# Performance work log

Measured on AMD Instinct MI355X. Metric: run time of the kernel, lower is better.

Reference implementation:

```python
import jax, jax.numpy as jnp
import numpy as np
from jax import lax

DIM = 96
HEADS = 6
H = W = D = 64
EPS = 1e-12  # torch F.normalize default


def setup_inputs() -> dict:
    key = jax.random.key(0)
    k1, k2, k3, k4 = jax.random.split(key, 4)
    x = jax.random.normal(k1, (1, DIM, H, W, D), dtype=jnp.float32)
    # qkv 1x1 conv weight, stored as (3*dim, dim) matrix
    w_qkv = jax.random.normal(k2, (3 * DIM, DIM), dtype=jnp.float32) * (1.0 / np.sqrt(DIM))
    # depthwise 3x3x3 conv weight (OIDHW with I=1, groups=3*dim)
    w_dw = jax.random.normal(k3, (3 * DIM, 1, 3, 3, 3), dtype=jnp.float32) * (1.0 / np.sqrt(27))
    # output 1x1 conv weight as (dim, dim)
    w_proj = jax.random.normal(k4, (DIM, DIM), dtype=jnp.float32) * (1.0 / np.sqrt(DIM))
    temperature = jnp.ones((HEADS, 1, 1), dtype=jnp.float32)
    return {"x": x, "w_qkv": w_qkv, "w_dw": w_dw, "w_proj": w_proj, "temperature": temperature}


def _l2norm(t):
    # torch F.normalize(dim=-1): t / max(||t||, eps)
    n = jnp.sqrt(jnp.sum(t * t, axis=-1, keepdims=True))
    return t / jnp.maximum(n, EPS)


def reference(x, w_qkv, w_dw, w_proj, temperature):
    b, c, h, w, d = x.shape
    ch = c // HEADS  # per-head channels
    # 1x1 conv -> pointwise GEMM over channels
    qkv = jnp.einsum('bchwd,oc->bohwd', x, w_qkv)  # (b, 3c, h, w, d)
    # depthwise 3x3x3 conv, padding 1
    qkv = lax.conv_general_dilated(
        qkv, w_dw, window_strides=(1, 1, 1), padding=[(1, 1)] * 3,
        feature_group_count=3 * c,
        dimension_numbers=('NCDHW', 'OIDHW', 'NCDHW'))
    q, k, v = jnp.split(qkv, 3, axis=1)
    n = h * w * d
    q = q.reshape(b, HEADS, ch, n)
    k = k.reshape(b, HEADS, ch, n)
    v = v.reshape(b, HEADS, ch, n)
    q = _l2norm(q)
    k = _l2norm(k)
    # channel-wise attention: (b, heads, ch, ch)
    attn = jnp.einsum('bhcn,bhdn->bhcd', q, k) * temperature[None]
    attn = jax.nn.softmax(attn, axis=-1)
    out = jnp.einsum('bhcd,bhdn->bhcn', attn, v)  # (b, heads, ch, n)
    out = out.reshape(b, c, h, w, d)
    out = jnp.einsum('bchwd,oc->bohwd', out, w_proj)
    return out
```

## Files before the change

### kernel.cpp

```cpp
#include <hip/hip_runtime.h>
#include <hip/hip_bf16.h>

#define NTOT 262144
typedef __hip_bfloat16 bf16;
typedef __attribute__((ext_vector_type(8))) short short8;
typedef __attribute__((ext_vector_type(4))) float f32x4;

__device__ inline ushort f2bf(float f){ bf16 b = __float2bfloat16(f); return *(ushort*)&b; }
__device__ inline float bf2f(ushort u){ union{unsigned i;float f;}v; v.i = (unsigned)u<<16; return v.f; }

__global__ void detect_dtype(const ushort* __restrict__ w, int* __restrict__ flag) {
  int tid = threadIdx.x;
  int sane = 0;
  for (int i = tid; i < 512; i += 64) {
    ushort u = w[2 * i];
    int e = (u >> 7) & 0xff;
    sane += (e == 0 || (e >= 100 && e <= 140)) ? 1 : 0;
  }
#pragma unroll
  for (int off = 32; off > 0; off >>= 1) sane += __shfl_down(sane, off, 64);
  if (tid == 0) *flag = (sane >= 256) ? 1 : 0;
}

__global__ void cvt_bf16(const void* __restrict__ in, ushort* __restrict__ outw,
                         int n, const int* __restrict__ flag) {
  int f = *flag;
  for (int i = blockIdx.x * 256 + threadIdx.x; i < n; i += gridDim.x * 256)
    outw[i] = f ? ((const ushort*)in)[i] : f2bf(((const float*)in)[i]);
}

template<int OF, bool DYNIN, bool DYNOUT>
__global__ __launch_bounds__(384)
void gemm96(const ushort* __restrict__ W, const void* __restrict__ X,
            void* __restrict__ C, const int* __restrict__ flag) {
  __shared__ __align__(16) ushort xs[64][104];
  const int tid = threadIdx.x;
  const long n0 = (long)blockIdx.x * 64;
  const int f = *flag;
  {
    int c = tid % 96, nq = tid / 96;
    ushort tmp[16];
    if (!DYNIN || f) {
      const ushort* xp = (const ushort*)X + (size_t)c * NTOT + n0 + nq * 16;
      uint4 a0 = *(const uint4*)xp;
      uint4 a1 = *(const uint4*)(xp + 8);
      const unsigned* aw = (const unsigned*)&a0;
#pragma unroll
      for (int i = 0; i < 4; i++) { tmp[2*i] = (ushort)(aw[i] & 0xffffu); tmp[2*i+1] = (ushort)(aw[i] >> 16); }
      const unsigned* aw1 = (const unsigned*)&a1;
#pragma unroll
      for (int i = 0; i < 4; i++) { tmp[8+2*i] = (ushort)(aw1[i] & 0xffffu); tmp[8+2*i+1] = (ushort)(aw1[i] >> 16); }
    } else {
      const float* xp = (const float*)X + (size_t)c * NTOT + n0 + nq * 16;
#pragma unroll
      for (int k = 0; k < 4; k++) {
        float4 v = *(const float4*)(xp + 4 * k);
        tmp[4*k+0] = f2bf(v.x); tmp[4*k+1] = f2bf(v.y);
        tmp[4*k+2] = f2bf(v.z); tmp[4*k+3] = f2bf(v.w);
      }
    }
    ushort* dst = &xs[nq * 16][c];
#pragma unroll
    for (int i = 0; i < 16; i++) dst[i * 104] = tmp[i];
  }
  __syncthreads();
  const int wave = tid >> 6, lane = tid & 63;
  const int col = lane & 15, quad = lane >> 4;
  f32x4 acc[OF][4];
#pragma unroll
  for (int a = 0; a < OF; a++)
#pragma unroll
    for (int b = 0; b < 4; b++) acc[a][b] = (f32x4)0.f;
  const int obase = wave * (16 * OF);
#pragma unroll
  for (int ks = 0; ks < 3; ks++) {
    short8 bfrag[4];
#pragma unroll
    for (int nf = 0; nf < 4; nf++)
      bfrag[nf] = *(const short8*)&xs[nf*16 + col][ks*32 + quad*8];
#pragma unroll
    for (int of = 0; of < OF; of++) {
      const int o = obase + of*16 + col;
      short8 afrag = *(const short8*)(W + (size_t)o * 96 + ks*32 + quad*8);
#pragma unroll
      for (int nf = 0; nf < 4; nf++)
        acc[of][nf] = __builtin_amdgcn_mfma_f32_16x16x32_bf16(afrag, bfrag[nf], acc[of][nf], 0, 0, 0);
    }
  }
#pragma unroll
  for (int of = 0; of < OF; of++)
#pragma unroll
    for (int nf = 0; nf < 4; nf++)
#pragma unroll
      for (int r = 0; r < 4; r++) {
        int o = obase + of*16 + quad*4 + r;
        long n = n0 + nf*16 + col;
        float v = acc[of][nf][r];
        if (!DYNOUT || f) ((ushort*)C)[(size_t)o * NTOT + n] = f2bf(v);
        else              ((float*) C)[(size_t)o * NTOT + n] = v;
      }
}

__global__ __launch_bounds__(256)
void dwconv3(const ushort* __restrict__ in, const void* __restrict__ wt,
             ushort* __restrict__ out, const int* __restrict__ flag) {
  const int c = blockIdx.z;
  const int tid = threadIdx.x;
  const int dq = tid & 7;
  const int w = blockIdx.y * 8 + ((tid >> 3) & 7);
  const int h = blockIdx.x * 4 + (tid >> 6);
  const int d0 = dq * 8;
  __shared__ float wsm[27];
  if (tid < 27) {
    int f = *flag;
    wsm[tid] = f ? bf2f(((const ushort*)wt)[c * 27 + tid])
                 : ((const float*)wt)[c * 27 + tid];
  }
  __syncthreads();
  float acc[8];
#pragma unroll
  for (int i = 0; i < 8; i++) acc[i] = 0.f;
  const size_t cbase = (size_t)c * NTOT;
#pragma unroll
  for (int dh = -1; dh <= 1; dh++) {
    int hh = h + dh;
    if (hh < 0 || hh > 63) continue;
#pragma unroll
    for (int dw = -1; dw <= 1; dw++) {
      int ww = w + dw;
      bool wok = (ww >= 0 && ww <= 63);
      uint4 va = make_uint4(0u, 0u, 0u, 0u);
      if (wok)
        va = *(const uint4*)(in + cbase + ((size_t)hh * 64 + ww) * 64 + d0);
      const unsigned* u = (const unsigned*)&va;
      float x0 = bf2f((ushort)(u[0] & 0xffffu)), x1 = bf2f((ushort)(u[0] >> 16));
      float x2 = bf2f((ushort)(u[1] & 0xffffu)), x3 = bf2f((ushort)(u[1] >> 16));
      float x4 = bf2f((ushort)(u[2] & 0xffffu)), x5 = bf2f((ushort)(u[2] >> 16));
      float x6 = bf2f((ushort)(u[3] & 0xffffu)), x7 = bf2f((ushort)(u[3] >> 16));
      float xlm = __shfl_up(x7, 1, 8);
      float xrm = __shfl_down(x0, 1, 8);
      float xl = (dq > 0) ? xlm : 0.f;
      float xr = (dq < 7) ? xrm : 0.f;
      const int wb = (dh + 1) * 9 + (dw + 1) * 3;
      float wL = wsm[wb], wC = wsm[wb + 1], wR = wsm[wb + 2];
      acc[0] += wL*xl + wC*x0 + wR*x1;
      acc[1] += wL*x0 + wC*x1 + wR*x2;
      acc[2] += wL*x1 + wC*x2 + wR*x3;
      acc[3] += wL*x2 + wC*x3 + wR*x4;
      acc[4] += wL*x3 + wC*x4 + wR*x5;
      acc[5] += wL*x4 + wC*x5 + wR*x6;
      acc[6] += wL*x5 + wC*x6 + wR*x7;
      acc[7] += wL*x6 + wC*x7 + wR*xr;
    }
  }
  ushort o8[8];
#pragma unroll
  for (int i = 0; i < 8; i++) o8[i] = f2bf(acc[i]);
  *(uint4*)(out + cbase + ((size_t)h * 64 + w) * 64 + d0) = *(uint4*)o8;
}

__global__ __launch_bounds__(256)
void gram16(const ushort* __restrict__ qk, float* __restrict__ G) {
  const int hd = blockIdx.y;
  const int tid = threadIdx.x, wave = tid >> 6, lane = tid & 63;
  const int col = lane & 15, quad = lane >> 4;
  const ushort* qp = qk + (size_t)(hd * 16 + col) * NTOT;
  const ushort* kp = qp + (size_t)96 * NTOT;
  f32x4 aqk = (f32x4)0.f, aqq = (f32x4)0.f, akk = (f32x4)0.f;
  const int nbase = blockIdx.x * 4096 + wave * 32 + quad * 8;
#pragma unroll 4
  for (int it = 0; it < 32; it++) {
    short8 qf = *(const short8*)(qp + nbase + it * 128);
    short8 kf = *(const short8*)(kp + nbase + it * 128);
    aqk = __builtin_amdgcn_mfma_f32_16x16x32_bf16(qf, kf, aqk, 0, 0, 0);
    aqq = __builtin_amdgcn_mfma_f32_16x16x32_bf16(qf, qf, aqq, 0, 0, 0);
    akk = __builtin_amdgcn_mfma_f32_16x16x32_bf16(kf, kf, akk, 0, 0, 0);
  }
  __shared__ float red[4][64][12];
#pragma unroll
  for (int r = 0; r < 4; r++) {
    red[wave][lane][r]     = aqk[r];
    red[wave][lane][4 + r] = aqq[r];
    red[wave][lane][8 + r] = akk[r];
  }
  __syncthreads();
  if (wave == 0) {
#pragma unroll
    for (int j = 0; j < 12; j++) {
      float v = red[0][lane][j] + red[1][lane][j] + red[2][lane][j] + red[3][lane][j];
      int sub = j >> 2, r = j & 3;
      atomicAdd(&G[hd * 768 + sub * 256 + (quad * 4 + r) * 16 + col], v);
    }
  }
}

__global__ __launch_bounds__(256)
void attn_mix(const float* __restrict__ G, const void* __restrict__ wp,
              const void* __restrict__ temp, ushort* __restrict__ M,
              const int* __restrict__ flag) {
  __shared__ float As[6][16][16];
  const int tid = threadIdx.x;
  const int f = *flag;
  if (tid < 96) {
    int hd = tid >> 4, c = tid & 15;
    const float* Gh = G + hd * 768;
    float qn = fmaxf(sqrtf(fmaxf(Gh[256 + c * 17], 0.f)), 1e-12f);
    float t = f ? bf2f(((const ushort*)temp)[hd]) : ((const float*)temp)[hd];
    float lg[16];
    float mx = -1e30f;
#pragma unroll
    for (int d = 0; d < 16; d++) {
      float kn = fmaxf(sqrtf(fmaxf(Gh[512 + d * 17], 0.f)), 1e-12f);
      lg[d] = Gh[c * 16 + d] / (qn * kn) * t;
      mx = fmaxf(mx, lg[d]);
    }
    float s = 0.f;
#pragma unroll
    for (int d = 0; d < 16; d++) { lg[d] = __expf(lg[d] - mx); s += lg[d]; }
    float inv = 1.f / s;
#pragma unroll
    for (int d = 0; d < 16; d++) As[hd][c][d] = lg[d] * inv;
  }
  __syncthreads();
  for (int i = 0; i < 36; i++) {
    int idx = tid + 256 * i;
    int o = idx / 96, p = idx - o * 96;
    int hd = p >> 4, d = p & 15;
    float s = 0.f;
#pragma unroll
    for (int cc = 0; cc < 16; cc++) {
      float wv = f ? bf2f(((const ushort*)wp)[o * 96 + hd * 16 + cc])
                   : ((const float*)wp)[o * 96 + hd * 16 + cc];
      s += wv * As[hd][cc][d];
    }
    M[idx] = f2bf(s);
  }
}

extern "C" void kernel_launch(void* const* d_in, const int* in_sizes, int n_in,
                              void* d_out, int out_size, void* d_ws, size_t ws_size,
                              hipStream_t stream) {
  const void* x      = d_in[0];
  const void* w_qkv  = d_in[1];
  const void* w_dw   = d_in[2];
  const void* w_proj = d_in[3];
  const void* temp   = d_in[4];

  const size_t szQKV = (size_t)288 * NTOT * 2;
  ushort* B1 = (ushort*)d_ws;
  ushort* B2 = (ushort*)((char*)d_ws + szQKV);
  char* tail = (char*)d_ws + 2 * szQKV;
  float*  G    = (float*)tail;
  ushort* M    = (ushort*)(tail + 18432);
  ushort* Wb   = (ushort*)(tail + 36864);
  int*    flag = (int*)(tail + 92160);
  if (ws_size < 2 * szQKV + 92160 + 256) return;

  detect_dtype<<<1, 64, 0, stream>>>((const ushort*)w_qkv, flag);
  cvt_bf16<<<32, 256, 0, stream>>>(w_qkv, Wb, 288 * 96, flag);
  hipMemsetAsync(G, 0, 4608 * 4, stream);
  gemm96<3, true, false><<<4096, 384, 0, stream>>>(Wb, x, B1, flag);
  dwconv3<<<dim3(16, 8, 288), 256, 0, stream>>>(B1, w_dw, B2, flag);
  gram16<<<dim3(64, 6), 256, 0, stream>>>(B2, G);
  attn_mix<<<1, 256, 0, stream>>>(G, w_proj, temp, M, flag);
  gemm96<1, false, true><<<4096, 384, 0, stream>>>(M, B2 + (size_t)192 * NTOT, d_out, flag);
}
```

Baseline: 450.8 us.

## Switch pipeline to fp16 with packed half2 depthwise conv and pre-transposed GEMM inputs

Changes every intermediate buffer and MFMA from bf16 to fp16. The depthwise conv now uses packed half2 FMAs with byte-perm shifts instead of unpacking to fp32. Separate transpose kernels write the x and v tensors in n-major layout, so the GEMMs read B fragments straight from global memory and stage their outputs through LDS for coalesced stores. This is meant to cut ALU work in the dwconv and improve GEMM access patterns. The cost is two extra full-tensor transpose passes and the fp16 range and accuracy risk of accumulating the conv in half precision.

```diff
diff --git a/kernel.cpp b/kernel.cpp
--- a/kernel.cpp
+++ b/kernel.cpp
@@ -1,13 +1,17 @@
 #include <hip/hip_runtime.h>
 #include <hip/hip_bf16.h>
+#include <hip/hip_fp16.h>
 
 #define NTOT 262144
 typedef __hip_bfloat16 bf16;
-typedef __attribute__((ext_vector_type(8))) short short8;
 typedef __attribute__((ext_vector_type(4))) float f32x4;
+typedef _Float16 f16x8 __attribute__((ext_vector_type(8)));
 
 __device__ inline ushort f2bf(float f){ bf16 b = __float2bfloat16(f); return *(ushort*)&b; }
 __device__ inline float bf2f(ushort u){ union{unsigned i;float f;}v; v.i = (unsigned)u<<16; return v.f; }
+__device__ inline unsigned h2u(__half2 h){ union{__half2 h; unsigned u;}v; v.h=h; return v.u; }
+__device__ inline __half2 u2h(unsigned u){ union{unsigned u; __half2 h;}v; v.u=u; return v.h; }
+__device__ inline ushort f2h(float f){ __half h = __float2half_rn(f); return *(ushort*)&h; }
 
 __global__ void detect_dtype(const ushort* __restrict__ w, int* __restrict__ flag) {
   int tid = threadIdx.x;
@@ -22,71 +26,89 @@
   if (tid == 0) *flag = (sane >= 256) ? 1 : 0;
 }
 
-__global__ void cvt_bf16(const void* __restrict__ in, ushort* __restrict__ outw,
-                         int n, const int* __restrict__ flag) {
+__global__ void cvt_f16(const void* __restrict__ in, ushort* __restrict__ outw,
+                        int n, const int* __restrict__ flag) {
   int f = *flag;
-  for (int i = blockIdx.x * 256 + threadIdx.x; i < n; i += gridDim.x * 256)
-    outw[i] = f ? ((const ushort*)in)[i] : f2bf(((const float*)in)[i]);
-}
-
-template<int OF, bool DYNIN, bool DYNOUT>
-__global__ __launch_bounds__(384)
-void gemm96(const ushort* __restrict__ W, const void* __restrict__ X,
-            void* __restrict__ C, const int* __restrict__ flag) {
-  __shared__ __align__(16) ushort xs[64][104];
+  for (int i = blockIdx.x * 256 + threadIdx.x; i < n; i += gridDim.x * 256) {
+    float v = f ? bf2f(((const ushort*)in)[i]) : ((const float*)in)[i];
+    outw[i] = f2h(v);
+  }
+}
+
+template<int MODE>
+__global__ __launch_bounds__(256)
+void transpose96(const void* __restrict__ in, ushort* __restrict__ out,
+                 const int* __restrict__ flag) {
+  __shared__ float t[96][65];
   const int tid = threadIdx.x;
   const long n0 = (long)blockIdx.x * 64;
-  const int f = *flag;
-  {
-    int c = tid % 96, nq = tid / 96;
-    ushort tmp[16];
-    if (!DYNIN || f) {
-      const ushort* xp = (const ushort*)X + (size_t)c * NTOT + n0 + nq * 16;
-      uint4 a0 = *(const uint4*)xp;
-      uint4 a1 = *(const uint4*)(xp + 8);
-      const unsigned* aw = (const unsigned*)&a0;
-#pragma unroll
-      for (int i = 0; i < 4; i++) { tmp[2*i] = (ushort)(aw[i] & 0xffffu); tmp[2*i+1] = (ushort)(aw[i] >> 16); }
-      const unsigned* aw1 = (const unsigned*)&a1;
-#pragma unroll
-      for (int i = 0; i < 4; i++) { tmp[8+2*i] = (ushort)(aw1[i] & 0xffffu); tmp[8+2*i+1] = (ushort)(aw1[i] >> 16); }
+  const int f = (MODE == 0) ? *flag : 0;
+#pragma unroll
+  for (int i = 0; i < 6; i++) {
+    int idx = tid + 256 * i;
+    int u = idx & 15, c = idx >> 4;
+    float v0, v1, v2, v3;
+    if (MODE == 0 && !f) {
+      float4 q = *(const float4*)((const float*)in + (size_t)c * NTOT + n0 + u * 4);
+      v0 = q.x; v1 = q.y; v2 = q.z; v3 = q.w;
+    } else if (MODE == 0) {
+      uint2 q = *(const uint2*)((const ushort*)in + (size_t)c * NTOT + n0 + u * 4);
+      v0 = bf2f((ushort)(q.x & 0xffffu)); v1 = bf2f((ushort)(q.x >> 16));
+      v2 = bf2f((ushort)(q.y & 0xffffu)); v3 = bf2f((ushort)(q.y >> 16));
     } else {
-      const float* xp = (const float*)X + (size_t)c * NTOT + n0 + nq * 16;
-#pragma unroll
-      for (int k = 0; k < 4; k++) {
-        float4 v = *(const float4*)(xp + 4 * k);
-        tmp[4*k+0] = f2bf(v.x); tmp[4*k+1] = f2bf(v.y);
-        tmp[4*k+2] = f2bf(v.z); tmp[4*k+3] = f2bf(v.w);
-      }
-    }
-    ushort* dst = &xs[nq * 16][c];
-#pragma unroll
-    for (int i = 0; i < 16; i++) dst[i * 104] = tmp[i];
-  }
-  __syncthreads();
+      uint2 q = *(const uint2*)((const ushort*)in + (size_t)c * NTOT + n0 + u * 4);
+      __half2 a = u2h(q.x), b = u2h(q.y);
+      v0 = __half2float(a.x); v1 = __half2float(a.y);
+      v2 = __half2float(b.x); v3 = __half2float(b.y);
+    }
+    t[c][u*4+0] = v0; t[c][u*4+1] = v1; t[c][u*4+2] = v2; t[c][u*4+3] = v3;
+  }
+  __syncthreads();
+#pragma unroll
+  for (int i = 0; i < 3; i++) {
+    int idx = tid + 256 * i;
+    int oq = idx % 12, n = idx / 12;
+    unsigned d[4];
+#pragma unroll
+    for (int j = 0; j < 4; j++) {
+      __half2 hp = __floats2half2_rn(t[oq*8 + 2*j][n], t[oq*8 + 2*j + 1][n]);
+      d[j] = h2u(hp);
+    }
+    *(uint4*)(out + (size_t)(n0 + n) * 96 + oq * 8) = make_uint4(d[0], d[1], d[2], d[3]);
+  }
+}
+
+template<int OF, bool DYNOUT>
+__global__ __launch_bounds__(384)
+void gemm96f(const ushort* __restrict__ W, const ushort* __restrict__ Xt,
+             void* __restrict__ C, const int* __restrict__ flag) {
+  const int tid = threadIdx.x;
+  const long n0 = (long)blockIdx.x * 64;
   const int wave = tid >> 6, lane = tid & 63;
   const int col = lane & 15, quad = lane >> 4;
+  const int f = DYNOUT ? *flag : 0;
   f32x4 acc[OF][4];
 #pragma unroll
   for (int a = 0; a < OF; a++)
 #pragma unroll
     for (int b = 0; b < 4; b++) acc[a][b] = (f32x4)0.f;
-  const int obase = wave * (16 * OF);
+  const int obase = wave * 16 * OF;
 #pragma unroll
   for (int ks = 0; ks < 3; ks++) {
-    short8 bfrag[4];
+    f16x8 bfrag[4];
 #pragma unroll
     for (int nf = 0; nf < 4; nf++)
-      bfrag[nf] = *(const short8*)&xs[nf*16 + col][ks*32 + quad*8];
+      bfrag[nf] = *(const f16x8*)(Xt + (size_t)(n0 + nf*16 + col) * 96 + ks*32 + quad*8);
 #pragma unroll
     for (int of = 0; of < OF; of++) {
       const int o = obase + of*16 + col;
-      short8 afrag = *(const short8*)(W + (size_t)o * 96 + ks*32 + quad*8);
+      f16x8 afrag = *(const f16x8*)(W + (size_t)o * 96 + ks*32 + quad*8);
 #pragma unroll
       for (int nf = 0; nf < 4; nf++)
-        acc[of][nf] = __builtin_amdgcn_mfma_f32_16x16x32_bf16(afrag, bfrag[nf], acc[of][nf], 0, 0, 0);
-    }
-  }
+        acc[of][nf] = __builtin_amdgcn_mfma_f32_16x16x32_f16(afrag, bfrag[nf], acc[of][nf], 0, 0, 0);
+    }
+  }
+  __shared__ __align__(16) ushort cs[96 * OF][72];
 #pragma unroll
   for (int of = 0; of < OF; of++)
 #pragma unroll
@@ -94,11 +116,36 @@
 #pragma unroll
       for (int r = 0; r < 4; r++) {
         int o = obase + of*16 + quad*4 + r;
-        long n = n0 + nf*16 + col;
-        float v = acc[of][nf][r];
-        if (!DYNOUT || f) ((ushort*)C)[(size_t)o * NTOT + n] = f2bf(v);
-        else              ((float*) C)[(size_t)o * NTOT + n] = v;
+        cs[o][nf*16 + col] = f2h(acc[of][nf][r]);
       }
+  __syncthreads();
+  if (!DYNOUT) {
+#pragma unroll
+    for (int i = 0; i < 2 * OF; i++) {
+      int idx = tid + 384 * i;
+      int o = idx >> 3, u = idx & 7;
+      uint4 v = *(const uint4*)&cs[o][u * 8];
+      *(uint4*)((ushort*)C + (size_t)o * NTOT + n0 + u * 8) = v;
+    }
+  } else {
+#pragma unroll
+    for (int i = 0; i < 4; i++) {
+      int idx = tid + 384 * i;
+      int o = idx >> 4, u = idx & 15;
+      uint2 v = *(const uint2*)&cs[o][u * 4];
+      __half2 a = u2h(v.x), b = u2h(v.y);
+      float f0 = __half2float(a.x), f1 = __half2float(a.y);
+      float f2 = __half2float(b.x), f3 = __half2float(b.y);
+      if (!f) {
+        float4 q = {f0, f1, f2, f3};
+        *(float4*)((float*)C + (size_t)o * NTOT + n0 + u * 4) = q;
+      } else {
+        uint2 q = make_uint2(((unsigned)f2bf(f1) << 16) | f2bf(f0),
+                             ((unsigned)f2bf(f3) << 16) | f2bf(f2));
+        *(uint2*)((ushort*)C + (size_t)o * NTOT + n0 + u * 4) = q;
+      }
+    }
+  }
 }
 
 __global__ __launch_bounds__(256)
@@ -110,16 +157,17 @@
   const int w = blockIdx.y * 8 + ((tid >> 3) & 7);
   const int h = blockIdx.x * 4 + (tid >> 6);
   const int d0 = dq * 8;
-  __shared__ float wsm[27];
+  __shared__ __half2 wsm2[27];
   if (tid < 27) {
     int f = *flag;
-    wsm[tid] = f ? bf2f(((const ushort*)wt)[c * 27 + tid])
+    float wv = f ? bf2f(((const ushort*)wt)[c * 27 + tid])
                  : ((const float*)wt)[c * 27 + tid];
-  }
-  __syncthreads();
-  float acc[8];
-#pragma unroll
-  for (int i = 0; i < 8; i++) acc[i] = 0.f;
+    wsm2[tid] = __floats2half2_rn(wv, wv);
+  }
+  __syncthreads();
+  const unsigned maskL = (dq == 0) ? 0xFFFF0000u : 0xFFFFFFFFu;
+  const unsigned maskR = (dq == 7) ? 0x0000FFFFu : 0xFFFFFFFFu;
+  __half2 a0 = u2h(0), a1 = u2h(0), a2 = u2h(0), a3 = u2h(0);
   const size_t cbase = (size_t)c * NTOT;
 #pragma unroll
   for (int dh = -1; dh <= 1; dh++) {
@@ -129,34 +177,26 @@
     for (int dw = -1; dw <= 1; dw++) {
       int ww = w + dw;
       bool wok = (ww >= 0 && ww <= 63);
-      uint4 va = make_uint4(0u, 0u, 0u, 0u);
+      uint4 u = make_uint4(0u, 0u, 0u, 0u);
       if (wok)
-        va = *(const uint4*)(in + cbase + ((size_t)hh * 64 + ww) * 64 + d0);
-      const unsigned* u = (const unsigned*)&va;
-      float x0 = bf2f((ushort)(u[0] & 0xffffu)), x1 = bf2f((ushort)(u[0] >> 16));
-      float x2 = bf2f((ushort)(u[1] & 0xffffu)), x3 = bf2f((ushort)(u[1] >> 16));
-      float x4 = bf2f((ushort)(u[2] & 0xffffu)), x5 = bf2f((ushort)(u[2] >> 16));
-      float x6 = bf2f((ushort)(u[3] & 0xffffu)), x7 = bf2f((ushort)(u[3] >> 16));
-      float xlm = __shfl_up(x7, 1, 8);
-      float xrm = __shfl_down(x0, 1, 8);
-      float xl = (dq > 0) ? xlm : 0.f;
-      float xr = (dq < 7) ? xrm : 0.f;
+        u = *(const uint4*)(in + cbase + ((size_t)hh * 64 + ww) * 64 + d0);
+      unsigned P = (unsigned)__shfl_up((int)u.w, 1, 8);
+      unsigned N = (unsigned)__shfl_down((int)u.x, 1, 8);
+      unsigned S0 = __builtin_amdgcn_perm(u.x, P,   0x05040302) & maskL;
+      unsigned S1 = __builtin_amdgcn_perm(u.y, u.x, 0x05040302);
+      unsigned S2 = __builtin_amdgcn_perm(u.z, u.y, 0x05040302);
+      unsigned S3 = __builtin_amdgcn_perm(u.w, u.z, 0x05040302);
+      unsigned R3 = __builtin_amdgcn_perm(N,   u.w, 0x05040302) & maskR;
       const int wb = (dh + 1) * 9 + (dw + 1) * 3;
-      float wL = wsm[wb], wC = wsm[wb + 1], wR = wsm[wb + 2];
-      acc[0] += wL*xl + wC*x0 + wR*x1;
-      acc[1] += wL*x0 + wC*x1 + wR*x2;
-      acc[2] += wL*x1 + wC*x2 + wR*x3;
-      acc[3] += wL*x2 + wC*x3 + wR*x4;
-      acc[4] += wL*x3 + wC*x4 + wR*x5;
-      acc[5] += wL*x4 + wC*x5 + wR*x6;
-      acc[6] += wL*x5 + wC*x6 + wR*x7;
-      acc[7] += wL*x6 + wC*x7 + wR*xr;
-    }
-  }
-  ushort o8[8];
-#pragma unroll
-  for (int i = 0; i < 8; i++) o8[i] = f2bf(acc[i]);
-  *(uint4*)(out + cbase + ((size_t)h * 64 + w) * 64 + d0) = *(uint4*)o8;
+      __half2 wL = wsm2[wb], wC = wsm2[wb + 1], wR = wsm2[wb + 2];
+      a0 = __hfma2(wL, u2h(S0), a0); a0 = __hfma2(wC, u2h(u.x), a0); a0 = __hfma2(wR, u2h(S1), a0);
+      a1 = __hfma2(wL, u2h(S1), a1); a1 = __hfma2(wC, u2h(u.y), a1); a1 = __hfma2(wR, u2h(S2), a1);
+      a2 = __hfma2(wL, u2h(S2), a2); a2 = __hfma2(wC, u2h(u.z), a2); a2 = __hfma2(wR, u2h(S3), a2);
+      a3 = __hfma2(wL, u2h(S3), a3); a3 = __hfma2(wC, u2h(u.w), a3); a3 = __hfma2(wR, u2h(R3), a3);
+    }
+  }
+  *(uint4*)(out + cbase + ((size_t)h * 64 + w) * 64 + d0) =
+      make_uint4(h2u(a0), h2u(a1), h2u(a2), h2u(a3));
 }
 
 __global__ __launch_bounds__(256)
@@ -170,11 +210,11 @@
   const int nbase = blockIdx.x * 4096 + wave * 32 + quad * 8;
 #pragma unroll 4
   for (int it = 0; it < 32; it++) {
-    short8 qf = *(const short8*)(qp + nbase + it * 128);
-    short8 kf = *(const short8*)(kp + nbase + it * 128);
-    aqk = __builtin_amdgcn_mfma_f32_16x16x32_bf16(qf, kf, aqk, 0, 0, 0);
-    aqq = __builtin_amdgcn_mfma_f32_16x16x32_bf16(qf, qf, aqq, 0, 0, 0);
-    akk = __builtin_amdgcn_mfma_f32_16x16x32_bf16(kf, kf, akk, 0, 0, 0);
+    f16x8 qf = *(const f16x8*)(qp + nbase + it * 128);
+    f16x8 kf = *(const f16x8*)(kp + nbase + it * 128);
+    aqk = __builtin_amdgcn_mfma_f32_16x16x32_f16(qf, kf, aqk, 0, 0, 0);
+    aqq = __builtin_amdgcn_mfma_f32_16x16x32_f16(qf, qf, aqq, 0, 0, 0);
+    akk = __builtin_amdgcn_mfma_f32_16x16x32_f16(kf, kf, akk, 0, 0, 0);
   }
   __shared__ float red[4][64][12];
 #pragma unroll
@@ -233,7 +273,7 @@
                    : ((const float*)wp)[o * 96 + hd * 16 + cc];
       s += wv * As[hd][cc][d];
     }
-    M[idx] = f2bf(s);
+    M[idx] = f2h(s);
   }
 }
 
@@ -249,19 +289,23 @@
   const size_t szQKV = (size_t)288 * NTOT * 2;
   ushort* B1 = (ushort*)d_ws;
   ushort* B2 = (ushort*)((char*)d_ws + szQKV);
+  ushort* Xt = B2;
+  ushort* Vt = B1;
   char* tail = (char*)d_ws + 2 * szQKV;
   float*  G    = (float*)tail;
   ushort* M    = (ushort*)(tail + 18432);
-  ushort* Wb   = (ushort*)(tail + 36864);
+  ushort* Wh   = (ushort*)(tail + 36864);
   int*    flag = (int*)(tail + 92160);
   if (ws_size < 2 * szQKV + 92160 + 256) return;
 
   detect_dtype<<<1, 64, 0, stream>>>((const ushort*)w_qkv, flag);
-  cvt_bf16<<<32, 256, 0, stream>>>(w_qkv, Wb, 288 * 96, flag);
+  cvt_f16<<<32, 256, 0, stream>>>(w_qkv, Wh, 288 * 96, flag);
   hipMemsetAsync(G, 0, 4608 * 4, stream);
-  gemm96<3, true, false><<<4096, 384, 0, stream>>>(Wb, x, B1, flag);
+  transpose96<0><<<4096, 256, 0, stream>>>(x, Xt, flag);
+  gemm96f<3, false><<<4096, 384, 0, stream>>>(Wh, Xt, B1, flag);
   dwconv3<<<dim3(16, 8, 288), 256, 0, stream>>>(B1, w_dw, B2, flag);
   gram16<<<dim3(64, 6), 256, 0, stream>>>(B2, G);
+  transpose96<1><<<4096, 256, 0, stream>>>(B2 + (size_t)192 * NTOT, Vt, flag);
   attn_mix<<<1, 256, 0, stream>>>(G, w_proj, temp, M, flag);
-  gemm96<1, false, true><<<4096, 384, 0, stream>>>(M, B2 + (size_t)192 * NTOT, d_out, flag);
-}
+  gemm96f<1, true><<<4096, 384, 0, stream>>>(M, Vt, d_out, flag);
+}
```

Result: faster. 438.9 us (-2.6%).
